# Kernel tuning notes

Hardware: AMD Instinct MI355X
Metric: run time of the kernel (lower is better)

Reference implementation:

```python
import jax, jax.numpy as jnp
import numpy as np

N, E, D, H, G = 50000, 800000, 256, 256, 64
EPS = 1e-5

def setup_inputs() -> dict:
    key = jax.random.key(0)
    ks = jax.random.split(key, 16)
    s_in = float(np.sqrt(2.0 / D))   # He fan_in init
    s_h = float(np.sqrt(2.0 / H))
    inp = {}
    inp['x'] = jax.random.normal(ks[0], (N, D), jnp.float32)
    inp['edge_index'] = jax.random.randint(ks[1], (2, E), 0, N)
    inp['batch'] = jnp.sort(jax.random.randint(ks[2], (N,), 0, G))
    inp['bn_in_g'] = jnp.ones((D,), jnp.float32)
    inp['bn_in_b'] = jnp.zeros((D,), jnp.float32)
    for i in range(3):
        fan = D if i == 0 else H
        inp[f'W{i}'] = jax.random.normal(ks[3 + i], (fan, H), jnp.float32) * float(np.sqrt(2.0 / fan))
        inp[f'b{i}'] = jnp.zeros((H,), jnp.float32)
        inp[f'bn{i}_g'] = jnp.ones((H,), jnp.float32)
        inp[f'bn{i}_b'] = jnp.zeros((H,), jnp.float32)
    inp['Wa1'] = jax.random.normal(ks[6], (H, H // 2), jnp.float32) * s_h
    inp['ba1'] = jnp.zeros((H // 2,), jnp.float32)
    inp['Wa2'] = jax.random.normal(ks[7], (H // 2, 1), jnp.float32) * float(np.sqrt(2.0 / (H // 2)))
    inp['ba2'] = jnp.zeros((1,), jnp.float32)
    inp['Wo'] = jax.random.normal(ks[8], (H, 2), jnp.float32) * s_h
    inp['bo'] = jnp.zeros((2,), jnp.float32)
    return inp


def _bn(x, g, b):
    # BatchNorm1d, batch statistics (training-mode normalization), biased var
    m = jnp.mean(x, axis=0)
    v = jnp.mean(jnp.square(x - m), axis=0)
    return (x - m) * jax.lax.rsqrt(v + EPS) * g + b


def _gcn(x, src, dst, W, b):
    h = x @ W  # [N, H]
    n = x.shape[0]
    deg = jax.ops.segment_sum(jnp.ones_like(src, x.dtype), dst, num_segments=n) + 1.0  # +1 self-loop
    dinv = jax.lax.rsqrt(deg)  # [N]
    msg = h[src] * (dinv[src] * dinv[dst])[:, None]          # gather + edgewise scale
    agg = jax.ops.segment_sum(msg, dst, num_segments=n)      # scatter-add at dst
    return agg + h * (dinv * dinv)[:, None] + b               # self-loop term fused


def reference(x, edge_index, batch, bn_in_g, bn_in_b,
              W0, b0, bn0_g, bn0_b, W1, b1, bn1_g, bn1_b, W2, b2, bn2_g, bn2_b,
              Wa1, ba1, Wa2, ba2, Wo, bo):
    src, dst = edge_index[0], edge_index[1]
    x = _bn(x, bn_in_g, bn_in_b)  # dropout = identity (eval)
    # layer 0
    xp = _bn(jax.nn.relu(_gcn(x, src, dst, W0, b0)), bn0_g, bn0_b)
    # layers 1..2 with residual
    for (W, b, g, bb) in ((W1, b1, bn1_g, bn1_b), (W2, b2, bn2_g, bn2_b)):
        xn = _bn(jax.nn.relu(_gcn(xp, src, dst, W, b)), g, bb)
        xp = xn + xp
    # attention over all nodes (softmax along node dim, as in source)
    scores = jax.nn.leaky_relu(xp @ Wa1 + ba1, 0.01) @ Wa2 + ba2  # [N,1]
    w = jax.nn.softmax(scores, axis=0)
    xw = xp * w
    cnt = jax.ops.segment_sum(jnp.ones((xp.shape[0],), xp.dtype), batch, num_segments=G)
    pooled = jax.ops.segment_sum(xw, batch, num_segments=G) / jnp.maximum(cnt, 1.0)[:, None]
    return pooled @ Wo + bo  # [G, 2]
```

## Files before the change

kernel.cpp:

```cpp
#include <hip/hip_runtime.h>

#define N_NODES 50000
#define N_EDGES 800000
#define DIM 256
#define NG 64
#define EPS_BN 1e-5f
#define NB_AGG 3125
#define NB_COL 512
#define NSPLIT 32

typedef _Float16 f16;
typedef _Float16 half8 __attribute__((ext_vector_type(8)));
typedef _Float16 half4 __attribute__((ext_vector_type(4)));
typedef float floatx4 __attribute__((ext_vector_type(4)));

__global__ __launch_bounds__(256) void col_stats_kernel(const float* __restrict__ X, int n,
                                                        float* __restrict__ part) {
    int c = threadIdx.x;
    float s = 0.f, q = 0.f;
    for (int i = blockIdx.x; i < n; i += gridDim.x) {
        float v = X[(size_t)i * DIM + c];
        s += v; q += v * v;
    }
    part[(size_t)blockIdx.x * 512 + c] = s;
    part[(size_t)blockIdx.x * 512 + DIM + c] = q;
}

__global__ __launch_bounds__(256) void reduce_stats_kernel(const float* __restrict__ part, int nrows,
                                                           float* __restrict__ p2) {
    int col = blockIdx.x * 256 + threadIdx.x;
    int chunk = (nrows + NSPLIT - 1) / NSPLIT;
    int r0 = blockIdx.y * chunk;
    int r1 = min(r0 + chunk, nrows);
    float t = 0.f;
    for (int r = r0; r < r1; r++) t += part[(size_t)r * 512 + col];
    p2[(size_t)blockIdx.y * 512 + col] = t;
}

__global__ void finalize_stats_kernel(const float* __restrict__ p2, float* __restrict__ mr, float inv_n) {
    int c = threadIdx.x;
    float s = 0.f, q = 0.f;
#pragma unroll
    for (int r = 0; r < NSPLIT; r++) {
        s += p2[(size_t)r * 512 + c];
        q += p2[(size_t)r * 512 + DIM + c];
    }
    float m = s * inv_n;
    float v = q * inv_n - m * m;
    mr[c] = m;
    mr[DIM + c] = rsqrtf(v + EPS_BN);
}

__global__ __launch_bounds__(256) void bn_apply_in_kernel(const float* __restrict__ Xin, f16* __restrict__ Af,
                                                          const float* __restrict__ mr, const float* __restrict__ g,
                                                          const float* __restrict__ b, int n) {
    int c = threadIdx.x;
    float mean = mr[c], rstd = mr[DIM + c], gg = g[c], bb = b[c];
    for (int i = blockIdx.x; i < n; i += gridDim.x) {
        size_t idx = (size_t)i * DIM + c;
        float v = Xin[idx];
        v = (v - mean) * rstd * gg + bb;
        Af[idx] = (f16)v;
    }
}

__global__ __launch_bounds__(256) void bn_apply_kernel(const f16* __restrict__ Cin, f16* __restrict__ Af,
                                                       const float* __restrict__ mr, const float* __restrict__ g,
                                                       const float* __restrict__ b, int n, int residual) {
    int c = threadIdx.x;
    float mean = mr[c], rstd = mr[DIM + c], gg = g[c], bb = b[c];
    for (int i = blockIdx.x; i < n; i += gridDim.x) {
        size_t idx = (size_t)i * DIM + c;
        float v = (float)Cin[idx];
        v = fmaxf(v, 0.f);
        v = (v - mean) * rstd * gg + bb;
        if (residual) v += (float)Af[idx];
        Af[idx] = (f16)v;
    }
}

__global__ void convert_wT_kernel(const float* __restrict__ W, f16* __restrict__ Wt, int K, int M) {
    int idx = blockIdx.x * 256 + threadIdx.x;
    if (idx < K * M) {
        int m = idx / K, k = idx % K;
        Wt[idx] = (f16)W[(size_t)k * M + m];
    }
}

__global__ void count_int_kernel(const int* __restrict__ idx, int n, int* __restrict__ cnt) {
    for (int i = blockIdx.x * blockDim.x + threadIdx.x; i < n; i += gridDim.x * blockDim.x)
        atomicAdd(&cnt[idx[i]], 1);
}

#define SCHUNK 2048
__global__ __launch_bounds__(256) void scan1_kernel(const int* __restrict__ cnt, int n,
                                                    int* __restrict__ outp, int* __restrict__ bsums,
                                                    float* __restrict__ dinv) {
    __shared__ int lds[256];
    int t = threadIdx.x;
    int base = blockIdx.x * SCHUNK + t * 8;
    int v[8]; int s = 0;
#pragma unroll
    for (int j = 0; j < 8; j++) {
        int id = base + j;
        int x = 0;
        if (id < n) { x = cnt[id]; dinv[id] = rsqrtf((float)x + 1.0f); }
        v[j] = s; s += x;
    }
    lds[t] = s; __syncthreads();
    for (int o = 1; o < 256; o <<= 1) {
        int add = (t >= o) ? lds[t - o] : 0;
        __syncthreads();
        lds[t] += add;
        __syncthreads();
    }
    int excl = lds[t] - s;
#pragma unroll
    for (int j = 0; j < 8; j++) { int id = base + j; if (id < n) outp[id] = excl + v[j]; }
    if (t == 255) bsums[blockIdx.x] = lds[255];
}

__global__ void scan2_kernel(int* bsums, int nb) {
    if (threadIdx.x == 0 && blockIdx.x == 0) {
        int r = 0;
        for (int i = 0; i < nb; i++) { int t = bsums[i]; bsums[i] = r; r += t; }
    }
}

__global__ void scan3_kernel(int* __restrict__ outp, const int* __restrict__ bsums, int n, int total) {
    int i = blockIdx.x * blockDim.x + threadIdx.x;
    if (i < n) outp[i] += bsums[i / SCHUNK];
    if (i == 0) outp[n] = total;
}

__global__ void scatter_kernel(const int* __restrict__ src, const int* __restrict__ dst, int ne,
                               const int* __restrict__ rowp, int* __restrict__ fill, int* __restrict__ ss) {
    for (int e = blockIdx.x * blockDim.x + threadIdx.x; e < ne; e += gridDim.x * blockDim.x) {
        int d = dst[e];
        int pos = rowp[d] + atomicAdd(&fill[d], 1);
        ss[pos] = src[e];
    }
}

__global__ void graph_bounds_kernel(const int* __restrict__ batch, int n, int* __restrict__ start) {
    int i = blockIdx.x * blockDim.x + threadIdx.x;
    if (i < n) {
        int b = batch[i];
        if (i == 0 || batch[i - 1] != b) start[b] = i;
    }
}

__global__ void graph_offsets2_kernel(const int* __restrict__ start, int* __restrict__ off, int* __restrict__ cnt) {
    if (threadIdx.x == 0 && blockIdx.x == 0) {
        int nxt = N_NODES;
        for (int g = NG - 1; g >= 0; --g) {
            int s = start[g];
            int o = (s < 0) ? nxt : s;
            off[g] = o;
            cnt[g] = nxt - o;
            nxt = o;
        }
    }
}

__global__ __launch_bounds__(256) void gcn_agg_kernel(const f16* __restrict__ h, const int* __restrict__ rowp,
                                                      const int* __restrict__ ss, const float* __restrict__ dinv,
                                                      const float* __restrict__ bias, f16* __restrict__ out,
                                                      float* __restrict__ part, int n) {
    int wave = threadIdx.x >> 6;
    int lane = threadIdx.x & 63;
    int c = lane * 4;
    float4 bv = *(const float4*)&bias[c];
    float s0 = 0.f, s1 = 0.f, s2 = 0.f, s3 = 0.f;
    float q0 = 0.f, q1 = 0.f, q2 = 0.f, q3 = 0.f;
    for (int row = blockIdx.x * 4 + wave; row < n; row += gridDim.x * 4) {
        float ax = 0.f, ay = 0.f, az = 0.f, aw = 0.f;
        int e0 = rowp[row], e1 = rowp[row + 1];
        int e = e0;
        for (; e + 3 < e1; e += 4) {
            int i0 = ss[e], i1 = ss[e + 1], i2 = ss[e + 2], i3 = ss[e + 3];
            half4 h0 = *(const half4*)&h[(size_t)i0 * DIM + c];
            half4 h1 = *(const half4*)&h[(size_t)i1 * DIM + c];
            half4 h2 = *(const half4*)&h[(size_t)i2 * DIM + c];
            half4 h3 = *(const half4*)&h[(size_t)i3 * DIM + c];
            ax += (float)h0[0] + (float)h1[0] + (float)h2[0] + (float)h3[0];
            ay += (float)h0[1] + (float)h1[1] + (float)h2[1] + (float)h3[1];
            az += (float)h0[2] + (float)h1[2] + (float)h2[2] + (float)h3[2];
            aw += (float)h0[3] + (float)h1[3] + (float)h2[3] + (float)h3[3];
        }
        for (; e < e1; e++) {
            int si = ss[e];
            half4 hv = *(const half4*)&h[(size_t)si * DIM + c];
            ax += (float)hv[0]; ay += (float)hv[1]; az += (float)hv[2]; aw += (float)hv[3];
        }
        float di = dinv[row];
        half4 hs = *(const half4*)&h[(size_t)row * DIM + c];
        float rx = di * (ax + (float)hs[0]) + bv.x;
        float ry = di * (ay + (float)hs[1]) + bv.y;
        float rz = di * (az + (float)hs[2]) + bv.z;
        float rw = di * (aw + (float)hs[3]) + bv.w;
        half4 o; o[0] = (f16)rx; o[1] = (f16)ry; o[2] = (f16)rz; o[3] = (f16)rw;
        *(half4*)&out[(size_t)row * DIM + c] = o;
        float t;
        t = fmaxf(rx, 0.f); s0 += t; q0 += t * t;
        t = fmaxf(ry, 0.f); s1 += t; q1 += t * t;
        t = fmaxf(rz, 0.f); s2 += t; q2 += t * t;
        t = fmaxf(rw, 0.f); s3 += t; q3 += t * t;
    }
    __shared__ float sred[4][64][4];
    __shared__ float qred[4][64][4];
    sred[wave][lane][0] = s0; sred[wave][lane][1] = s1; sred[wave][lane][2] = s2; sred[wave][lane][3] = s3;
    qred[wave][lane][0] = q0; qred[wave][lane][1] = q1; qred[wave][lane][2] = q2; qred[wave][lane][3] = q3;
    __syncthreads();
    if (wave == 0) {
        size_t base = (size_t)blockIdx.x * 512;
        float4 a = make_float4(0.f, 0.f, 0.f, 0.f), qv = make_float4(0.f, 0.f, 0.f, 0.f);
#pragma unroll
        for (int ww = 0; ww < 4; ww++) {
            a.x += sred[ww][lane][0]; a.y += sred[ww][lane][1]; a.z += sred[ww][lane][2]; a.w += sred[ww][lane][3];
            qv.x += qred[ww][lane][0]; qv.y += qred[ww][lane][1]; qv.z += qred[ww][lane][2]; qv.w += qred[ww][lane][3];
        }
        *(float4*)&part[base + c] = a;
        *(float4*)&part[base + DIM + c] = qv;
    }
}

#define BM 128
#define BN 128
#define BK 32
#define LDP 40
__global__ __launch_bounds__(256) void gemm_f16_kernel(const f16* __restrict__ Af, const f16* __restrict__ Wt,
                                                       f16* __restrict__ C, const float* __restrict__ scale,
                                                       int n, int K, int M) {
    __shared__ __align__(16) f16 As[BM * LDP];
    __shared__ __align__(16) f16 Bs[BN * LDP];
    int tid = threadIdx.x;
    int wave = tid >> 6, lane = tid & 63;
    int wm = wave >> 1, wn = wave & 1;
    int q = lane >> 4, l16 = lane & 15;
    int bm = blockIdx.x * BM, bn = blockIdx.y * BN;
    floatx4 acc[4][4] = {};
    for (int k0 = 0; k0 < K; k0 += BK) {
#pragma unroll
        for (int rr = 0; rr < 2; rr++) {
            int cidx = tid + rr * 256;
            int row = cidx >> 2, off = (cidx & 3) * 8;
            int arow = bm + row; if (arow >= n) arow = n - 1;
            *(float4*)&As[row * LDP + off] = *(const float4*)&Af[(size_t)arow * K + k0 + off];
            int brow = bn + row;
            *(float4*)&Bs[row * LDP + off] = *(const float4*)&Wt[(size_t)brow * K + k0 + off];
        }
        __syncthreads();
        half8 af[4], bf[4];
#pragma unroll
        for (int i = 0; i < 4; i++) af[i] = *(half8*)&As[(wm * 64 + i * 16 + l16) * LDP + q * 8];
#pragma unroll
        for (int j = 0; j < 4; j++) bf[j] = *(half8*)&Bs[(wn * 64 + j * 16 + l16) * LDP + q * 8];
#pragma unroll
        for (int i = 0; i < 4; i++)
#pragma unroll
            for (int j = 0; j < 4; j++)
                acc[i][j] = __builtin_amdgcn_mfma_f32_16x16x32_f16(af[i], bf[j], acc[i][j], 0, 0, 0);
        __syncthreads();
    }
#pragma unroll
    for (int i = 0; i < 4; i++) {
#pragma unroll
        for (int r = 0; r < 4; r++) {
            int row = bm + wm * 64 + i * 16 + q * 4 + r;
            if (row < n) {
                float sc = scale ? scale[row] : 1.0f;
#pragma unroll
                for (int j = 0; j < 4; j++) {
                    int col = bn + wn * 64 + j * 16 + l16;
                    C[(size_t)row * M + col] = (f16)(acc[i][j][r] * sc);
                }
            }
        }
    }
}

__global__ __launch_bounds__(256) void gemm_attn_kernel(const f16* __restrict__ Af, const f16* __restrict__ Wt,
                                                        const float* __restrict__ ba1, const float* __restrict__ Wa2,
                                                        const float* __restrict__ ba2, float* __restrict__ score,
                                                        int n, int K) {
    __shared__ __align__(16) f16 As[BM * LDP];
    __shared__ __align__(16) f16 Bs[128 * LDP];
    __shared__ float scred[128][2];
    int tid = threadIdx.x;
    int wave = tid >> 6, lane = tid & 63;
    int wm = wave >> 1, wn = wave & 1;
    int q = lane >> 4, l16 = lane & 15;
    int bm = blockIdx.x * BM;
    floatx4 acc[4][4] = {};
    for (int k0 = 0; k0 < K; k0 += BK) {
#pragma unroll
        for (int rr = 0; rr < 2; rr++) {
            int cidx = tid + rr * 256;
            int row = cidx >> 2, off = (cidx & 3) * 8;
            int arow = bm + row; if (arow >= n) arow = n - 1;
            *(float4*)&As[row * LDP + off] = *(const float4*)&Af[(size_t)arow * K + k0 + off];
            *(float4*)&Bs[row * LDP + off] = *(const float4*)&Wt[(size_t)row * K + k0 + off];
        }
        __syncthreads();
        half8 af[4], bf[4];
#pragma unroll
        for (int i = 0; i < 4; i++) af[i] = *(half8*)&As[(wm * 64 + i * 16 + l16) * LDP + q * 8];
#pragma unroll
        for (int j = 0; j < 4; j++) bf[j] = *(half8*)&Bs[(wn * 64 + j * 16 + l16) * LDP + q * 8];
#pragma unroll
        for (int i = 0; i < 4; i++)
#pragma unroll
            for (int j = 0; j < 4; j++)
                acc[i][j] = __builtin_amdgcn_mfma_f32_16x16x32_f16(af[i], bf[j], acc[i][j], 0, 0, 0);
        __syncthreads();
    }
    float ba1v[4], wa2v[4];
#pragma unroll
    for (int j = 0; j < 4; j++) {
        int col = wn * 64 + j * 16 + l16;
        ba1v[j] = ba1[col];
        wa2v[j] = Wa2[col];
    }
#pragma unroll
    for (int i = 0; i < 4; i++)
#pragma unroll
        for (int r = 0; r < 4; r++) {
            float p = 0.f;
#pragma unroll
            for (int j = 0; j < 4; j++) {
                float v = acc[i][j][r] + ba1v[j];
                v = (v > 0.f) ? v : 0.01f * v;
                p += v * wa2v[j];
            }
#pragma unroll
            for (int o = 1; o < 16; o <<= 1) p += __shfl_xor(p, o);
            if (l16 == 0) scred[wm * 64 + i * 16 + q * 4 + r][wn] = p;
        }
    __syncthreads();
    if (tid < 128) {
        int grow = bm + tid;
        if (grow < n) score[grow] = scred[tid][0] + scred[tid][1] + ba2[0];
    }
}

__global__ __launch_bounds__(256) void reduce_max_kernel(const float* __restrict__ s, int n, float* __restrict__ part) {
    __shared__ float lds[256];
    float m = -3.0e38f;
    for (int i = blockIdx.x * 256 + threadIdx.x; i < n; i += gridDim.x * 256) m = fmaxf(m, s[i]);
    lds[threadIdx.x] = m; __syncthreads();
    for (int o = 128; o > 0; o >>= 1) {
        if (threadIdx.x < o) lds[threadIdx.x] = fmaxf(lds[threadIdx.x], lds[threadIdx.x + o]);
        __syncthreads();
    }
    if (threadIdx.x == 0) part[blockIdx.x] = lds[0];
}

__global__ __launch_bounds__(256) void reduce_sumexp_kernel(const float* __restrict__ s, int n,
                                                            const float* __restrict__ part_max,
                                                            float* __restrict__ part_sum) {
    __shared__ float lds[256];
    int t = threadIdx.x;
    lds[t] = part_max[t]; __syncthreads();
    for (int o = 128; o > 0; o >>= 1) {
        if (t < o) lds[t] = fmaxf(lds[t], lds[t + o]);
        __syncthreads();
    }
    float mx = lds[0];
    __syncthreads();
    float acc = 0.f;
    for (int i = blockIdx.x * 256 + t; i < n; i += gridDim.x * 256) acc += expf(s[i] - mx);
    lds[t] = acc; __syncthreads();
    for (int o = 128; o > 0; o >>= 1) {
        if (t < o) lds[t] += lds[t + o];
        __syncthreads();
    }
    if (t == 0) part_sum[blockIdx.x] = lds[0];
}

__global__ __launch_bounds__(256) void pool_kernel(const f16* __restrict__ Af, const float* __restrict__ score,
                                                   const int* __restrict__ offs, const int* __restrict__ cnts,
                                                   const float* __restrict__ part_max, float* __restrict__ pooled) {
    __shared__ float lds[256];
    int c = threadIdx.x;
    lds[c] = part_max[c]; __syncthreads();
    for (int o = 128; o > 0; o >>= 1) {
        if (c < o) lds[c] = fmaxf(lds[c], lds[c + o]);
        __syncthreads();
    }
    float mx = lds[0];
    int g = blockIdx.x;
    int st = offs[g], cn = cnts[g];
    float acc = 0.f;
    for (int i = (int)blockIdx.y; i < cn; i += 32) {
        int i1 = i + 8, i2 = i + 16, i3 = i + 24;
        float s0 = score[st + i];
        float s1 = (i1 < cn) ? score[st + i1] : -3.0e38f;
        float s2 = (i2 < cn) ? score[st + i2] : -3.0e38f;
        float s3 = (i3 < cn) ? score[st + i3] : -3.0e38f;
        float a0 = (float)Af[(size_t)(st + i) * DIM + c];
        float a1 = (i1 < cn) ? (float)Af[(size_t)(st + i1) * DIM + c] : 0.f;
        float a2 = (i2 < cn) ? (float)Af[(size_t)(st + i2) * DIM + c] : 0.f;
        float a3 = (i3 < cn) ? (float)Af[(size_t)(st + i3) * DIM + c] : 0.f;
        acc += a0 * expf(s0 - mx) + a1 * expf(s1 - mx) + a2 * expf(s2 - mx) + a3 * expf(s3 - mx);
    }
    atomicAdd(&pooled[g * DIM + c], acc);
}

__global__ __launch_bounds__(256) void out_kernel(const float* __restrict__ pooled, const int* __restrict__ cnt,
                                                  const float* __restrict__ part_sum, const float* __restrict__ Wo,
                                                  const float* __restrict__ bo, float* __restrict__ out) {
    __shared__ float l0[256], l1[256];
    int g = blockIdx.x, c = threadIdx.x;
    l0[c] = part_sum[c]; __syncthreads();
    for (int o = 128; o > 0; o >>= 1) {
        if (c < o) l0[c] += l0[c + o];
        __syncthreads();
    }
    float denom = l0[0];
    __syncthreads();
    float scale = 1.f / (denom * fmaxf((float)cnt[g], 1.f));
    float v = pooled[g * DIM + c] * scale;
    l0[c] = v * Wo[c * 2];
    l1[c] = v * Wo[c * 2 + 1];
    __syncthreads();
    for (int o = 128; o > 0; o >>= 1) {
        if (c < o) { l0[c] += l0[c + o]; l1[c] += l1[c + o]; }
        __syncthreads();
    }
    if (c == 0) { out[g * 2] = l0[0] + bo[0]; out[g * 2 + 1] = l1[0] + bo[1]; }
}

extern "C" void kernel_launch(void* const* d_in, const int* in_sizes, int n_in,
                              void* d_out, int out_size, void* d_ws, size_t ws_size,
                              hipStream_t stream) {
    const float* x       = (const float*)d_in[0];
    const int*   ei      = (const int*)d_in[1];
    const int*   batch   = (const int*)d_in[2];
    const float* bn_in_g = (const float*)d_in[3];
    const float* bn_in_b = (const float*)d_in[4];
    const float* Ws[3]   = {(const float*)d_in[5],  (const float*)d_in[9],  (const float*)d_in[13]};
    const float* bs[3]   = {(const float*)d_in[6],  (const float*)d_in[10], (const float*)d_in[14]};
    const float* gs[3]   = {(const float*)d_in[7],  (const float*)d_in[11], (const float*)d_in[15]};
    const float* bbs[3]  = {(const float*)d_in[8],  (const float*)d_in[12], (const float*)d_in[16]};
    const float* Wa1 = (const float*)d_in[17];
    const float* ba1 = (const float*)d_in[18];
    const float* Wa2 = (const float*)d_in[19];
    const float* ba2 = (const float*)d_in[20];
    const float* Wo  = (const float*)d_in[21];
    const float* bo  = (const float*)d_in[22];

    char* w = (char*)d_ws;
    size_t off = 0;
    auto alloc = [&](size_t bytes) -> void* {
        void* p = w + off;
        off += (bytes + 255) & ~(size_t)255;
        return p;
    };
    int*   deg     = (int*)alloc((size_t)N_NODES * 4);
    int*   fill    = (int*)alloc((size_t)N_NODES * 4);
    float* pooled  = (float*)alloc((size_t)NG * DIM * 4);
    size_t zero_span = off;
    float* stats_part = (float*)alloc((size_t)NB_AGG * 512 * 4);
    float* stats_p2   = (float*)alloc((size_t)NSPLIT * 512 * 4);
    f16*   Afh  = (f16*)alloc((size_t)N_NODES * DIM * 2);
    f16*   Bh   = (f16*)alloc((size_t)N_NODES * DIM * 2);
    f16*   Ch   = (f16*)alloc((size_t)N_NODES * DIM * 2);
    f16*   Wt[3];
    for (int l = 0; l < 3; l++) Wt[l] = (f16*)alloc((size_t)DIM * DIM * 2);
    f16*   Wa1t = (f16*)alloc((size_t)128 * DIM * 2);
    int* sorted_src = (int*)alloc((size_t)N_EDGES * 4);
    float* dinv = (float*)alloc((size_t)N_NODES * 4);
    int* rowp   = (int*)alloc((size_t)(N_NODES + 1) * 4);
    float* score = (float*)alloc((size_t)N_NODES * 4);
    float* mr    = (float*)alloc(512 * 4);
    int* bsums   = (int*)alloc(64 * 4);
    float* part_max = (float*)alloc(256 * 4);
    float* part_sum = (float*)alloc(256 * 4);
    int* gstart  = (int*)alloc(64 * 4);
    int* cnt_g   = (int*)alloc(64 * 4);
    int* off_g   = (int*)alloc(64 * 4);

    const int* src = ei;
    const int* dst = ei + N_EDGES;
    const int NSCAN = (N_NODES + SCHUNK - 1) / SCHUNK;

    hipMemsetAsync(d_ws, 0, zero_span, stream);
    hipMemsetAsync(gstart, 0xff, 64 * 4, stream);

    count_int_kernel<<<3125, 256, 0, stream>>>(dst, N_EDGES, deg);
    scan1_kernel<<<NSCAN, 256, 0, stream>>>(deg, N_NODES, rowp, bsums, dinv);
    scan2_kernel<<<1, 64, 0, stream>>>(bsums, NSCAN);
    scan3_kernel<<<(N_NODES + 255) / 256, 256, 0, stream>>>(rowp, bsums, N_NODES, N_EDGES);
    scatter_kernel<<<3125, 256, 0, stream>>>(src, dst, N_EDGES, rowp, fill, sorted_src);

    graph_bounds_kernel<<<(N_NODES + 255) / 256, 256, 0, stream>>>(batch, N_NODES, gstart);
    graph_offsets2_kernel<<<1, 64, 0, stream>>>(gstart, off_g, cnt_g);

    for (int l = 0; l < 3; l++)
        convert_wT_kernel<<<DIM * DIM / 256, 256, 0, stream>>>(Ws[l], Wt[l], DIM, DIM);
    convert_wT_kernel<<<128 * DIM / 256, 256, 0, stream>>>(Wa1, Wa1t, DIM, 128);

    col_stats_kernel<<<NB_COL, 256, 0, stream>>>(x, N_NODES, stats_part);
    reduce_stats_kernel<<<dim3(2, NSPLIT), 256, 0, stream>>>(stats_part, NB_COL, stats_p2);
    finalize_stats_kernel<<<1, 256, 0, stream>>>(stats_p2, mr, 1.f / N_NODES);
    bn_apply_in_kernel<<<1024, 256, 0, stream>>>(x, Afh, mr, bn_in_g, bn_in_b, N_NODES);

    dim3 ggrid((N_NODES + BM - 1) / BM, DIM / BN);
    for (int l = 0; l < 3; l++) {
        gemm_f16_kernel<<<ggrid, 256, 0, stream>>>(Afh, Wt[l], Bh, dinv, N_NODES, DIM, DIM);
        gcn_agg_kernel<<<NB_AGG, 256, 0, stream>>>(Bh, rowp, sorted_src, dinv, bs[l], Ch, stats_part, N_NODES);
        reduce_stats_kernel<<<dim3(2, NSPLIT), 256, 0, stream>>>(stats_part, NB_AGG, stats_p2);
        finalize_stats_kernel<<<1, 256, 0, stream>>>(stats_p2, mr, 1.f / N_NODES);
        bn_apply_kernel<<<1024, 256, 0, stream>>>(Ch, Afh, mr, gs[l], bbs[l], N_NODES, (l > 0) ? 1 : 0);
    }

    gemm_attn_kernel<<<(N_NODES + BM - 1) / BM, 256, 0, stream>>>(Afh, Wa1t, ba1, Wa2, ba2, score, N_NODES, DIM);
    reduce_max_kernel<<<256, 256, 0, stream>>>(score, N_NODES, part_max);
    reduce_sumexp_kernel<<<256, 256, 0, stream>>>(score, N_NODES, part_max, part_sum);

    pool_kernel<<<dim3(NG, 8), 256, 0, stream>>>(Afh, score, off_g, cnt_g, part_max, pooled);
    out_kernel<<<NG, 256, 0, stream>>>(pooled, cnt_g, part_sum, Wo, bo, (float*)d_out);
}
```

Before: 765.0 us.

## Fuse BN apply into GEMM prologues and collapse many small launches

The batch-norm apply (with ReLU and residual add) now runs inside the GEMM's A-tile load, so the separate bn_apply passes over the node features disappear. Stats reduction and finalize merge into one kernel that uses a last-block atomic counter, and the softmax max and sum move into the attention GEMM and the pool kernel via an atomic max key and an atomic exp-sum. Weight conversion, degree count and graph bounds each become a single launch, scan2 is folded into scan3, and the aggregation gather is unrolled by eight with readfirstlane indices. The result is fewer launches and less memory traffic, at the cost of recomputing the BN transform in every GEMM column block and relying on grid-wide atomics.

After: 743.4 us. -2.8%, faster.

```diff
diff --git a/kernel.cpp b/kernel.cpp
--- a/kernel.cpp
+++ b/kernel.cpp
@@ -14,6 +14,9 @@
 typedef _Float16 half4 __attribute__((ext_vector_type(4)));
 typedef float floatx4 __attribute__((ext_vector_type(4)));
 
+__device__ __forceinline__ int fkey(float f) { int i = __float_as_int(f); return (i >= 0) ? i : (i ^ 0x7fffffff); }
+__device__ __forceinline__ float keyf(int k) { return __int_as_float((k >= 0) ? k : (k ^ 0x7fffffff)); }
+
 __global__ __launch_bounds__(256) void col_stats_kernel(const float* __restrict__ X, int n,
                                                         float* __restrict__ part) {
     int c = threadIdx.x;
@@ -26,8 +29,10 @@
     part[(size_t)blockIdx.x * 512 + DIM + c] = q;
 }
 
-__global__ __launch_bounds__(256) void reduce_stats_kernel(const float* __restrict__ part, int nrows,
-                                                           float* __restrict__ p2) {
+__global__ __launch_bounds__(256) void reduce_finalize_kernel(const float* __restrict__ part, int nrows,
+                                                              float* __restrict__ p2, int* __restrict__ counter,
+                                                              const float* __restrict__ g, const float* __restrict__ b,
+                                                              float* __restrict__ affine, float inv_n) {
     int col = blockIdx.x * 256 + threadIdx.x;
     int chunk = (nrows + NSPLIT - 1) / NSPLIT;
     int r0 = blockIdx.y * chunk;
@@ -35,61 +40,59 @@
     float t = 0.f;
     for (int r = r0; r < r1; r++) t += part[(size_t)r * 512 + col];
     p2[(size_t)blockIdx.y * 512 + col] = t;
-}
-
-__global__ void finalize_stats_kernel(const float* __restrict__ p2, float* __restrict__ mr, float inv_n) {
-    int c = threadIdx.x;
-    float s = 0.f, q = 0.f;
-#pragma unroll
-    for (int r = 0; r < NSPLIT; r++) {
-        s += p2[(size_t)r * 512 + c];
-        q += p2[(size_t)r * 512 + DIM + c];
-    }
-    float m = s * inv_n;
-    float v = q * inv_n - m * m;
-    mr[c] = m;
-    mr[DIM + c] = rsqrtf(v + EPS_BN);
-}
-
-__global__ __launch_bounds__(256) void bn_apply_in_kernel(const float* __restrict__ Xin, f16* __restrict__ Af,
-                                                          const float* __restrict__ mr, const float* __restrict__ g,
-                                                          const float* __restrict__ b, int n) {
-    int c = threadIdx.x;
-    float mean = mr[c], rstd = mr[DIM + c], gg = g[c], bb = b[c];
-    for (int i = blockIdx.x; i < n; i += gridDim.x) {
-        size_t idx = (size_t)i * DIM + c;
-        float v = Xin[idx];
-        v = (v - mean) * rstd * gg + bb;
-        Af[idx] = (f16)v;
-    }
-}
-
-__global__ __launch_bounds__(256) void bn_apply_kernel(const f16* __restrict__ Cin, f16* __restrict__ Af,
-                                                       const float* __restrict__ mr, const float* __restrict__ g,
-                                                       const float* __restrict__ b, int n, int residual) {
-    int c = threadIdx.x;
-    float mean = mr[c], rstd = mr[DIM + c], gg = g[c], bb = b[c];
-    for (int i = blockIdx.x; i < n; i += gridDim.x) {
-        size_t idx = (size_t)i * DIM + c;
-        float v = (float)Cin[idx];
-        v = fmaxf(v, 0.f);
-        v = (v - mean) * rstd * gg + bb;
-        if (residual) v += (float)Af[idx];
-        Af[idx] = (f16)v;
-    }
-}
-
-__global__ void convert_wT_kernel(const float* __restrict__ W, f16* __restrict__ Wt, int K, int M) {
+    __threadfence();
+    __shared__ int lastf;
+    if (threadIdx.x == 0) lastf = (atomicAdd(counter, 1) == 2 * NSPLIT - 1) ? 1 : 0;
+    __syncthreads();
+    if (lastf) {
+        __threadfence();
+        int c = threadIdx.x;
+        float s = 0.f, q = 0.f;
+#pragma unroll
+        for (int r = 0; r < NSPLIT; r++) {
+            s += p2[(size_t)r * 512 + c];
+            q += p2[(size_t)r * 512 + DIM + c];
+        }
+        float m = s * inv_n;
+        float v = q * inv_n - m * m;
+        float rstd = rsqrtf(v + EPS_BN);
+        float A = rstd * g[c];
+        affine[c] = A;
+        affine[DIM + c] = b[c] - m * A;
+    }
+}
+
+__global__ void convert_all_kernel(const float* __restrict__ W0, const float* __restrict__ W1,
+                                   const float* __restrict__ W2, const float* __restrict__ Wa1,
+                                   f16* __restrict__ T0, f16* __restrict__ T1,
+                                   f16* __restrict__ T2, f16* __restrict__ T3) {
     int idx = blockIdx.x * 256 + threadIdx.x;
-    if (idx < K * M) {
-        int m = idx / K, k = idx % K;
-        Wt[idx] = (f16)W[(size_t)k * M + m];
-    }
-}
-
-__global__ void count_int_kernel(const int* __restrict__ idx, int n, int* __restrict__ cnt) {
-    for (int i = blockIdx.x * blockDim.x + threadIdx.x; i < n; i += gridDim.x * blockDim.x)
-        atomicAdd(&cnt[idx[i]], 1);
+    if (idx < 196608) {
+        int w = idx >> 16, r = idx & 65535;
+        const float* W = (w == 0) ? W0 : (w == 1) ? W1 : W2;
+        f16* T = (w == 0) ? T0 : (w == 1) ? T1 : T2;
+        int m = r >> 8, k = r & 255;
+        T[r] = (f16)W[(size_t)k * 256 + m];
+    } else {
+        int r = idx - 196608;
+        int m = r >> 8, k = r & 255;
+        T3[r] = (f16)Wa1[(size_t)k * 128 + m];
+    }
+}
+
+__global__ void count_bounds_kernel(const int* __restrict__ dst, int ne, int* __restrict__ cnt,
+                                    const int* __restrict__ batch, int n, int* __restrict__ start) {
+    int gb = blockIdx.x;
+    if (gb < NB_AGG) {
+        for (int i = gb * 256 + threadIdx.x; i < ne; i += NB_AGG * 256)
+            atomicAdd(&cnt[dst[i]], 1);
+    } else {
+        int i = (gb - NB_AGG) * 256 + threadIdx.x;
+        if (i < n) {
+            int b = batch[i];
+            if (i == 0 || batch[i - 1] != b) start[b] = i;
+        }
+    }
 }
 
 #define SCHUNK 2048
@@ -120,16 +123,14 @@
     if (t == 255) bsums[blockIdx.x] = lds[255];
 }
 
-__global__ void scan2_kernel(int* bsums, int nb) {
-    if (threadIdx.x == 0 && blockIdx.x == 0) {
-        int r = 0;
-        for (int i = 0; i < nb; i++) { int t = bsums[i]; bsums[i] = r; r += t; }
-    }
-}
-
 __global__ void scan3_kernel(int* __restrict__ outp, const int* __restrict__ bsums, int n, int total) {
     int i = blockIdx.x * blockDim.x + threadIdx.x;
-    if (i < n) outp[i] += bsums[i / SCHUNK];
+    if (i < n) {
+        int k = i / SCHUNK;
+        int pref = 0;
+        for (int j = 0; j < k; j++) pref += bsums[j];
+        outp[i] += pref;
+    }
     if (i == 0) outp[n] = total;
 }
 
@@ -142,15 +143,8 @@
     }
 }
 
-__global__ void graph_bounds_kernel(const int* __restrict__ batch, int n, int* __restrict__ start) {
-    int i = blockIdx.x * blockDim.x + threadIdx.x;
-    if (i < n) {
-        int b = batch[i];
-        if (i == 0 || batch[i - 1] != b) start[b] = i;
-    }
-}
-
-__global__ void graph_offsets2_kernel(const int* __restrict__ start, int* __restrict__ off, int* __restrict__ cnt) {
+__global__ void graph_offsets2_kernel(const int* __restrict__ start, int* __restrict__ off, int* __restrict__ cnt,
+                                      int* __restrict__ maxkey) {
     if (threadIdx.x == 0 && blockIdx.x == 0) {
         int nxt = N_NODES;
         for (int g = NG - 1; g >= 0; --g) {
@@ -160,6 +154,7 @@
             cnt[g] = nxt - o;
             nxt = o;
         }
+        maxkey[0] = 0x80000000;
     }
 }
 
@@ -171,46 +166,61 @@
     int lane = threadIdx.x & 63;
     int c = lane * 4;
     float4 bv = *(const float4*)&bias[c];
-    float s0 = 0.f, s1 = 0.f, s2 = 0.f, s3 = 0.f;
-    float q0 = 0.f, q1 = 0.f, q2 = 0.f, q3 = 0.f;
+    float s0a = 0.f, s1a = 0.f, s2a = 0.f, s3a = 0.f;
+    float q0a = 0.f, q1a = 0.f, q2a = 0.f, q3a = 0.f;
     for (int row = blockIdx.x * 4 + wave; row < n; row += gridDim.x * 4) {
         float ax = 0.f, ay = 0.f, az = 0.f, aw = 0.f;
         int e0 = rowp[row], e1 = rowp[row + 1];
         int e = e0;
-        for (; e + 3 < e1; e += 4) {
-            int i0 = ss[e], i1 = ss[e + 1], i2 = ss[e + 2], i3 = ss[e + 3];
-            half4 h0 = *(const half4*)&h[(size_t)i0 * DIM + c];
-            half4 h1 = *(const half4*)&h[(size_t)i1 * DIM + c];
-            half4 h2 = *(const half4*)&h[(size_t)i2 * DIM + c];
-            half4 h3 = *(const half4*)&h[(size_t)i3 * DIM + c];
-            ax += (float)h0[0] + (float)h1[0] + (float)h2[0] + (float)h3[0];
-            ay += (float)h0[1] + (float)h1[1] + (float)h2[1] + (float)h3[1];
-            az += (float)h0[2] + (float)h1[2] + (float)h2[2] + (float)h3[2];
-            aw += (float)h0[3] + (float)h1[3] + (float)h2[3] + (float)h3[3];
+        for (; e + 8 <= e1; e += 8) {
+            int i0 = __builtin_amdgcn_readfirstlane(ss[e + 0]);
+            int i1 = __builtin_amdgcn_readfirstlane(ss[e + 1]);
+            int i2 = __builtin_amdgcn_readfirstlane(ss[e + 2]);
+            int i3 = __builtin_amdgcn_readfirstlane(ss[e + 3]);
+            int i4 = __builtin_amdgcn_readfirstlane(ss[e + 4]);
+            int i5 = __builtin_amdgcn_readfirstlane(ss[e + 5]);
+            int i6 = __builtin_amdgcn_readfirstlane(ss[e + 6]);
+            int i7 = __builtin_amdgcn_readfirstlane(ss[e + 7]);
+            half4 v0 = *(const half4*)&h[((size_t)i0 << 8) + c];
+            half4 v1 = *(const half4*)&h[((size_t)i1 << 8) + c];
+            half4 v2 = *(const half4*)&h[((size_t)i2 << 8) + c];
+            half4 v3 = *(const half4*)&h[((size_t)i3 << 8) + c];
+            half4 v4 = *(const half4*)&h[((size_t)i4 << 8) + c];
+            half4 v5 = *(const half4*)&h[((size_t)i5 << 8) + c];
+            half4 v6 = *(const half4*)&h[((size_t)i6 << 8) + c];
+            half4 v7 = *(const half4*)&h[((size_t)i7 << 8) + c];
+            ax += ((float)v0[0] + (float)v1[0]) + ((float)v2[0] + (float)v3[0]) +
+                  ((float)v4[0] + (float)v5[0]) + ((float)v6[0] + (float)v7[0]);
+            ay += ((float)v0[1] + (float)v1[1]) + ((float)v2[1] + (float)v3[1]) +
+                  ((float)v4[1] + (float)v5[1]) + ((float)v6[1] + (float)v7[1]);
+            az += ((float)v0[2] + (float)v1[2]) + ((float)v2[2] + (float)v3[2]) +
+                  ((float)v4[2] + (float)v5[2]) + ((float)v6[2] + (float)v7[2]);
+            aw += ((float)v0[3] + (float)v1[3]) + ((float)v2[3] + (float)v3[3]) +
+                  ((float)v4[3] + (float)v5[3]) + ((float)v6[3] + (float)v7[3]);
         }
         for (; e < e1; e++) {
-            int si = ss[e];
-            half4 hv = *(const half4*)&h[(size_t)si * DIM + c];
+            int si = __builtin_amdgcn_readfirstlane(ss[e]);
+            half4 hv = *(const half4*)&h[((size_t)si << 8) + c];
             ax += (float)hv[0]; ay += (float)hv[1]; az += (float)hv[2]; aw += (float)hv[3];
         }
         float di = dinv[row];
-        half4 hs = *(const half4*)&h[(size_t)row * DIM + c];
+        half4 hs = *(const half4*)&h[((size_t)row << 8) + c];
         float rx = di * (ax + (float)hs[0]) + bv.x;
         float ry = di * (ay + (float)hs[1]) + bv.y;
         float rz = di * (az + (float)hs[2]) + bv.z;
         float rw = di * (aw + (float)hs[3]) + bv.w;
         half4 o; o[0] = (f16)rx; o[1] = (f16)ry; o[2] = (f16)rz; o[3] = (f16)rw;
-        *(half4*)&out[(size_t)row * DIM + c] = o;
+        *(half4*)&out[((size_t)row << 8) + c] = o;
         float t;
-        t = fmaxf(rx, 0.f); s0 += t; q0 += t * t;
-        t = fmaxf(ry, 0.f); s1 += t; q1 += t * t;
-        t = fmaxf(rz, 0.f); s2 += t; q2 += t * t;
-        t = fmaxf(rw, 0.f); s3 += t; q3 += t * t;
+        t = fmaxf(rx, 0.f); s0a += t; q0a += t * t;
+        t = fmaxf(ry, 0.f); s1a += t; q1a += t * t;
+        t = fmaxf(rz, 0.f); s2a += t; q2a += t * t;
+        t = fmaxf(rw, 0.f); s3a += t; q3a += t * t;
     }
     __shared__ float sred[4][64][4];
     __shared__ float qred[4][64][4];
-    sred[wave][lane][0] = s0; sred[wave][lane][1] = s1; sred[wave][lane][2] = s2; sred[wave][lane][3] = s3;
-    qred[wave][lane][0] = q0; qred[wave][lane][1] = q1; qred[wave][lane][2] = q2; qred[wave][lane][3] = q3;
+    sred[wave][lane][0] = s0a; sred[wave][lane][1] = s1a; sred[wave][lane][2] = s2a; sred[wave][lane][3] = s3a;
+    qred[wave][lane][0] = q0a; qred[wave][lane][1] = q1a; qred[wave][lane][2] = q2a; qred[wave][lane][3] = q3a;
     __syncthreads();
     if (wave == 0) {
         size_t base = (size_t)blockIdx.x * 512;
@@ -229,38 +239,69 @@
 #define BN 128
 #define BK 32
 #define LDP 40
-__global__ __launch_bounds__(256) void gemm_f16_kernel(const f16* __restrict__ Af, const f16* __restrict__ Wt,
-                                                       f16* __restrict__ C, const float* __restrict__ scale,
-                                                       int n, int K, int M) {
+__global__ __launch_bounds__(256) void gemm_fused_kernel(const float* __restrict__ Xf32, const f16* __restrict__ Ch,
+                                                         const f16* __restrict__ Aold, f16* __restrict__ Afout,
+                                                         const float* __restrict__ affine,
+                                                         const f16* __restrict__ Wt, f16* __restrict__ Cout,
+                                                         const float* __restrict__ scale, int n, int K, int M) {
     __shared__ __align__(16) f16 As[BM * LDP];
     __shared__ __align__(16) f16 Bs[BN * LDP];
+    __shared__ float sA[256], sB[256];
     int tid = threadIdx.x;
+    if (tid < 256) { sA[tid] = affine[tid]; sB[tid] = affine[256 + tid]; }
     int wave = tid >> 6, lane = tid & 63;
     int wm = wave >> 1, wn = wave & 1;
     int q = lane >> 4, l16 = lane & 15;
     int bm = blockIdx.x * BM, bn = blockIdx.y * BN;
+    int kc = (tid & 3) * 8;
+    int writer = (Afout != nullptr) && (blockIdx.y == 0);
     floatx4 acc[4][4] = {};
+    __syncthreads();
     for (int k0 = 0; k0 < K; k0 += BK) {
+        float a8[8], b8[8];
+#pragma unroll
+        for (int j = 0; j < 8; j++) { a8[j] = sA[k0 + kc + j]; b8[j] = sB[k0 + kc + j]; }
 #pragma unroll
         for (int rr = 0; rr < 2; rr++) {
             int cidx = tid + rr * 256;
-            int row = cidx >> 2, off = (cidx & 3) * 8;
+            int row = cidx >> 2;
             int arow = bm + row; if (arow >= n) arow = n - 1;
-            *(float4*)&As[row * LDP + off] = *(const float4*)&Af[(size_t)arow * K + k0 + off];
+            float v[8];
+            if (Xf32) {
+                float4 x0 = *(const float4*)&Xf32[(size_t)arow * K + k0 + kc];
+                float4 x1 = *(const float4*)&Xf32[(size_t)arow * K + k0 + kc + 4];
+                v[0] = x0.x; v[1] = x0.y; v[2] = x0.z; v[3] = x0.w;
+                v[4] = x1.x; v[5] = x1.y; v[6] = x1.z; v[7] = x1.w;
+            } else {
+                half8 ch = *(const half8*)&Ch[(size_t)arow * K + k0 + kc];
+#pragma unroll
+                for (int j = 0; j < 8; j++) v[j] = fmaxf((float)ch[j], 0.f);
+            }
+            half8 af;
+            if (Aold) {
+                half8 ao = *(const half8*)&Aold[(size_t)arow * K + k0 + kc];
+#pragma unroll
+                for (int j = 0; j < 8; j++) af[j] = (f16)(v[j] * a8[j] + b8[j] + (float)ao[j]);
+            } else {
+#pragma unroll
+                for (int j = 0; j < 8; j++) af[j] = (f16)(v[j] * a8[j] + b8[j]);
+            }
+            *(float4*)&As[row * LDP + kc] = *(float4*)&af;
+            if (writer && bm + row < n) *(half8*)&Afout[(size_t)arow * K + k0 + kc] = af;
             int brow = bn + row;
-            *(float4*)&Bs[row * LDP + off] = *(const float4*)&Wt[(size_t)brow * K + k0 + off];
-        }
-        __syncthreads();
-        half8 af[4], bf[4];
-#pragma unroll
-        for (int i = 0; i < 4; i++) af[i] = *(half8*)&As[(wm * 64 + i * 16 + l16) * LDP + q * 8];
-#pragma unroll
-        for (int j = 0; j < 4; j++) bf[j] = *(half8*)&Bs[(wn * 64 + j * 16 + l16) * LDP + q * 8];
+            *(float4*)&Bs[row * LDP + kc] = *(const float4*)&Wt[(size_t)brow * K + k0 + kc];
+        }
+        __syncthreads();
+        half8 afr[4], bfr[4];
+#pragma unroll
+        for (int i = 0; i < 4; i++) afr[i] = *(half8*)&As[(wm * 64 + i * 16 + l16) * LDP + q * 8];
+#pragma unroll
+        for (int j = 0; j < 4; j++) bfr[j] = *(half8*)&Bs[(wn * 64 + j * 16 + l16) * LDP + q * 8];
 #pragma unroll
         for (int i = 0; i < 4; i++)
 #pragma unroll
             for (int j = 0; j < 4; j++)
-                acc[i][j] = __builtin_amdgcn_mfma_f32_16x16x32_f16(af[i], bf[j], acc[i][j], 0, 0, 0);
+                acc[i][j] = __builtin_amdgcn_mfma_f32_16x16x32_f16(afr[i], bfr[j], acc[i][j], 0, 0, 0);
         __syncthreads();
     }
 #pragma unroll
@@ -269,50 +310,66 @@
         for (int r = 0; r < 4; r++) {
             int row = bm + wm * 64 + i * 16 + q * 4 + r;
             if (row < n) {
-                float sc = scale ? scale[row] : 1.0f;
+                float sc = scale[row];
 #pragma unroll
                 for (int j = 0; j < 4; j++) {
                     int col = bn + wn * 64 + j * 16 + l16;
-                    C[(size_t)row * M + col] = (f16)(acc[i][j][r] * sc);
+                    Cout[(size_t)row * M + col] = (f16)(acc[i][j][r] * sc);
                 }
             }
         }
     }
 }
 
-__global__ __launch_bounds__(256) void gemm_attn_kernel(const f16* __restrict__ Af, const f16* __restrict__ Wt,
+__global__ __launch_bounds__(256) void gemm_attn_kernel(const f16* __restrict__ Ch, const f16* __restrict__ Aold,
+                                                        f16* __restrict__ Afout, const float* __restrict__ affine,
+                                                        const f16* __restrict__ Wt,
                                                         const float* __restrict__ ba1, const float* __restrict__ Wa2,
                                                         const float* __restrict__ ba2, float* __restrict__ score,
-                                                        int n, int K) {
+                                                        int* __restrict__ maxkey, int n, int K) {
     __shared__ __align__(16) f16 As[BM * LDP];
     __shared__ __align__(16) f16 Bs[128 * LDP];
+    __shared__ float sA[256], sB[256];
     __shared__ float scred[128][2];
     int tid = threadIdx.x;
+    if (tid < 256) { sA[tid] = affine[tid]; sB[tid] = affine[256 + tid]; }
     int wave = tid >> 6, lane = tid & 63;
     int wm = wave >> 1, wn = wave & 1;
     int q = lane >> 4, l16 = lane & 15;
     int bm = blockIdx.x * BM;
+    int kc = (tid & 3) * 8;
     floatx4 acc[4][4] = {};
+    __syncthreads();
     for (int k0 = 0; k0 < K; k0 += BK) {
+        float a8[8], b8[8];
+#pragma unroll
+        for (int j = 0; j < 8; j++) { a8[j] = sA[k0 + kc + j]; b8[j] = sB[k0 + kc + j]; }
 #pragma unroll
         for (int rr = 0; rr < 2; rr++) {
             int cidx = tid + rr * 256;
-            int row = cidx >> 2, off = (cidx & 3) * 8;
+            int row = cidx >> 2;
             int arow = bm + row; if (arow >= n) arow = n - 1;
-            *(float4*)&As[row * LDP + off] = *(const float4*)&Af[(size_t)arow * K + k0 + off];
-            *(float4*)&Bs[row * LDP + off] = *(const float4*)&Wt[(size_t)row * K + k0 + off];
-        }
-        __syncthreads();
-        half8 af[4], bf[4];
-#pragma unroll
-        for (int i = 0; i < 4; i++) af[i] = *(half8*)&As[(wm * 64 + i * 16 + l16) * LDP + q * 8];
-#pragma unroll
-        for (int j = 0; j < 4; j++) bf[j] = *(half8*)&Bs[(wn * 64 + j * 16 + l16) * LDP + q * 8];
+            half8 ch = *(const half8*)&Ch[(size_t)arow * K + k0 + kc];
+            half8 ao = *(const half8*)&Aold[(size_t)arow * K + k0 + kc];
+            half8 af;
+#pragma unroll
+            for (int j = 0; j < 8; j++)
+                af[j] = (f16)(fmaxf((float)ch[j], 0.f) * a8[j] + b8[j] + (float)ao[j]);
+            *(float4*)&As[row * LDP + kc] = *(float4*)&af;
+            if (bm + row < n) *(half8*)&Afout[(size_t)arow * K + k0 + kc] = af;
+            *(float4*)&Bs[row * LDP + kc] = *(const float4*)&Wt[(size_t)row * K + k0 + kc];
+        }
+        __syncthreads();
+        half8 afr[4], bfr[4];
+#pragma unroll
+        for (int i = 0; i < 4; i++) afr[i] = *(half8*)&As[(wm * 64 + i * 16 + l16) * LDP + q * 8];
+#pragma unroll
+        for (int j = 0; j < 4; j++) bfr[j] = *(half8*)&Bs[(wn * 64 + j * 16 + l16) * LDP + q * 8];
 #pragma unroll
         for (int i = 0; i < 4; i++)
 #pragma unroll
             for (int j = 0; j < 4; j++)
-                acc[i][j] = __builtin_amdgcn_mfma_f32_16x16x32_f16(af[i], bf[j], acc[i][j], 0, 0, 0);
+                acc[i][j] = __builtin_amdgcn_mfma_f32_16x16x32_f16(afr[i], bfr[j], acc[i][j], 0, 0, 0);
         __syncthreads();
     }
     float ba1v[4], wa2v[4];
@@ -338,88 +395,54 @@
             if (l16 == 0) scred[wm * 64 + i * 16 + q * 4 + r][wn] = p;
         }
     __syncthreads();
+    __shared__ float mred[128];
     if (tid < 128) {
         int grow = bm + tid;
-        if (grow < n) score[grow] = scred[tid][0] + scred[tid][1] + ba2[0];
-    }
-}
-
-__global__ __launch_bounds__(256) void reduce_max_kernel(const float* __restrict__ s, int n, float* __restrict__ part) {
-    __shared__ float lds[256];
-    float m = -3.0e38f;
-    for (int i = blockIdx.x * 256 + threadIdx.x; i < n; i += gridDim.x * 256) m = fmaxf(m, s[i]);
-    lds[threadIdx.x] = m; __syncthreads();
-    for (int o = 128; o > 0; o >>= 1) {
-        if (threadIdx.x < o) lds[threadIdx.x] = fmaxf(lds[threadIdx.x], lds[threadIdx.x + o]);
-        __syncthreads();
-    }
-    if (threadIdx.x == 0) part[blockIdx.x] = lds[0];
-}
-
-__global__ __launch_bounds__(256) void reduce_sumexp_kernel(const float* __restrict__ s, int n,
-                                                            const float* __restrict__ part_max,
-                                                            float* __restrict__ part_sum) {
-    __shared__ float lds[256];
-    int t = threadIdx.x;
-    lds[t] = part_max[t]; __syncthreads();
-    for (int o = 128; o > 0; o >>= 1) {
-        if (t < o) lds[t] = fmaxf(lds[t], lds[t + o]);
-        __syncthreads();
-    }
-    float mx = lds[0];
-    __syncthreads();
-    float acc = 0.f;
-    for (int i = blockIdx.x * 256 + t; i < n; i += gridDim.x * 256) acc += expf(s[i] - mx);
-    lds[t] = acc; __syncthreads();
-    for (int o = 128; o > 0; o >>= 1) {
-        if (t < o) lds[t] += lds[t + o];
-        __syncthreads();
-    }
-    if (t == 0) part_sum[blockIdx.x] = lds[0];
+        float sc = scred[tid][0] + scred[tid][1] + ba2[0];
+        if (grow < n) score[grow] = sc; else sc = -3.0e38f;
+        mred[tid] = sc;
+    }
+    __syncthreads();
+    for (int o = 64; o > 0; o >>= 1) {
+        if (tid < o && tid + o < 128) mred[tid] = fmaxf(mred[tid], mred[tid + o]);
+        __syncthreads();
+    }
+    if (tid == 0) atomicMax(maxkey, fkey(mred[0]));
 }
 
 __global__ __launch_bounds__(256) void pool_kernel(const f16* __restrict__ Af, const float* __restrict__ score,
                                                    const int* __restrict__ offs, const int* __restrict__ cnts,
-                                                   const float* __restrict__ part_max, float* __restrict__ pooled) {
-    __shared__ float lds[256];
+                                                   const int* __restrict__ maxkey, float* __restrict__ expsum,
+                                                   float* __restrict__ pooled) {
+    float mx = keyf(maxkey[0]);
     int c = threadIdx.x;
-    lds[c] = part_max[c]; __syncthreads();
-    for (int o = 128; o > 0; o >>= 1) {
-        if (c < o) lds[c] = fmaxf(lds[c], lds[c + o]);
-        __syncthreads();
-    }
-    float mx = lds[0];
     int g = blockIdx.x;
     int st = offs[g], cn = cnts[g];
-    float acc = 0.f;
+    float acc = 0.f, esum = 0.f;
     for (int i = (int)blockIdx.y; i < cn; i += 32) {
         int i1 = i + 8, i2 = i + 16, i3 = i + 24;
         float s0 = score[st + i];
         float s1 = (i1 < cn) ? score[st + i1] : -3.0e38f;
         float s2 = (i2 < cn) ? score[st + i2] : -3.0e38f;
         float s3 = (i3 < cn) ? score[st + i3] : -3.0e38f;
+        float e0 = expf(s0 - mx), e1 = expf(s1 - mx), e2 = expf(s2 - mx), e3 = expf(s3 - mx);
         float a0 = (float)Af[(size_t)(st + i) * DIM + c];
         float a1 = (i1 < cn) ? (float)Af[(size_t)(st + i1) * DIM + c] : 0.f;
         float a2 = (i2 < cn) ? (float)Af[(size_t)(st + i2) * DIM + c] : 0.f;
         float a3 = (i3 < cn) ? (float)Af[(size_t)(st + i3) * DIM + c] : 0.f;
-        acc += a0 * expf(s0 - mx) + a1 * expf(s1 - mx) + a2 * expf(s2 - mx) + a3 * expf(s3 - mx);
+        acc += a0 * e0 + a1 * e1 + a2 * e2 + a3 * e3;
+        esum += (e0 + e1) + (e2 + e3);
     }
     atomicAdd(&pooled[g * DIM + c], acc);
+    if (c == 0) atomicAdd(expsum, esum);
 }
 
 __global__ __launch_bounds__(256) void out_kernel(const float* __restrict__ pooled, const int* __restrict__ cnt,
-                                                  const float* __restrict__ part_sum, const float* __restrict__ Wo,
+                                                  const float* __restrict__ expsum, const float* __restrict__ Wo,
                                                   const float* __restrict__ bo, float* __restrict__ out) {
     __shared__ float l0[256], l1[256];
     int g = blockIdx.x, c = threadIdx.x;
-    l0[c] = part_sum[c]; __syncthreads();
-    for (int o = 128; o > 0; o >>= 1) {
-        if (c < o) l0[c] += l0[c + o];
-        __syncthreads();
-    }
-    float denom = l0[0];
-    __syncthreads();
-    float scale = 1.f / (denom * fmaxf((float)cnt[g], 1.f));
+    float scale = 1.f / (expsum[0] * fmaxf((float)cnt[g], 1.f));
     float v = pooled[g * DIM + c] * scale;
     l0[c] = v * Wo[c * 2];
     l1[c] = v * Wo[c * 2 + 1];
@@ -460,12 +483,16 @@
     int*   deg     = (int*)alloc((size_t)N_NODES * 4);
     int*   fill    = (int*)alloc((size_t)N_NODES * 4);
     float* pooled  = (float*)alloc((size_t)NG * DIM * 4);
+    int*   counters = (int*)alloc(4 * 4);
+    float* expsum  = (float*)alloc(4);
     size_t zero_span = off;
     float* stats_part = (float*)alloc((size_t)NB_AGG * 512 * 4);
     float* stats_p2   = (float*)alloc((size_t)NSPLIT * 512 * 4);
-    f16*   Afh  = (f16*)alloc((size_t)N_NODES * DIM * 2);
+    float* affine  = (float*)alloc(512 * 4);
+    f16*   AfA  = (f16*)alloc((size_t)N_NODES * DIM * 2);
+    f16*   AfB  = (f16*)alloc((size_t)N_NODES * DIM * 2);
     f16*   Bh   = (f16*)alloc((size_t)N_NODES * DIM * 2);
-    f16*   Ch   = (f16*)alloc((size_t)N_NODES * DIM * 2);
+    f16*   Chb  = (f16*)alloc((size_t)N_NODES * DIM * 2);
     f16*   Wt[3];
     for (int l = 0; l < 3; l++) Wt[l] = (f16*)alloc((size_t)DIM * DIM * 2);
     f16*   Wa1t = (f16*)alloc((size_t)128 * DIM * 2);
@@ -473,10 +500,8 @@
     float* dinv = (float*)alloc((size_t)N_NODES * 4);
     int* rowp   = (int*)alloc((size_t)(N_NODES + 1) * 4);
     float* score = (float*)alloc((size_t)N_NODES * 4);
-    float* mr    = (float*)alloc(512 * 4);
     int* bsums   = (int*)alloc(64 * 4);
-    float* part_max = (float*)alloc(256 * 4);
-    float* part_sum = (float*)alloc(256 * 4);
+    int* maxkey  = (int*)alloc(16);
     int* gstart  = (int*)alloc(64 * 4);
     int* cnt_g   = (int*)alloc(64 * 4);
     int* off_g   = (int*)alloc(64 * 4);
@@ -484,41 +509,40 @@
     const int* src = ei;
     const int* dst = ei + N_EDGES;
     const int NSCAN = (N_NODES + SCHUNK - 1) / SCHUNK;
+    const float inv_n = 1.f / N_NODES;
 
     hipMemsetAsync(d_ws, 0, zero_span, stream);
     hipMemsetAsync(gstart, 0xff, 64 * 4, stream);
 
-    count_int_kernel<<<3125, 256, 0, stream>>>(dst, N_EDGES, deg);
+    count_bounds_kernel<<<NB_AGG + 196, 256, 0, stream>>>(dst, N_EDGES, deg, batch, N_NODES, gstart);
     scan1_kernel<<<NSCAN, 256, 0, stream>>>(deg, N_NODES, rowp, bsums, dinv);
-    scan2_kernel<<<1, 64, 0, stream>>>(bsums, NSCAN);
     scan3_kernel<<<(N_NODES + 255) / 256, 256, 0, stream>>>(rowp, bsums, N_NODES, N_EDGES);
-    scatter_kernel<<<3125, 256, 0, stream>>>(src, dst, N_EDGES, rowp, fill, sorted_src);
-
-    graph_bounds_kernel<<<(N_NODES + 255) / 256, 256, 0, stream>>>(batch, N_NODES, gstart);
-    graph_offsets2_kernel<<<1, 64, 0, stream>>>(gstart, off_g, cnt_g);
-
-    for (int l = 0; l < 3; l++)
-        convert_wT_kernel<<<DIM * DIM / 256, 256, 0, stream>>>(Ws[l], Wt[l], DIM, DIM);
-    convert_wT_kernel<<<128 * DIM / 256, 256, 0, stream>>>(Wa1, Wa1t, DIM, 128);
+    scatter_kernel<<<NB_AGG, 256, 0, stream>>>(src, dst, N_EDGES, rowp, fill, sorted_src);
+    graph_offsets2_kernel<<<1, 64, 0, stream>>>(gstart, off_g, cnt_g, maxkey);
+
+    convert_all_kernel<<<896, 256, 0, stream>>>(Ws[0], Ws[1], Ws[2], Wa1, Wt[0], Wt[1], Wt[2], Wa1t);
 
     col_stats_kernel<<<NB_COL, 256, 0, stream>>>(x, N_NODES, stats_part);
-    reduce_stats_kernel<<<dim3(2, NSPLIT), 256, 0, stream>>>(stats_part, NB_COL, stats_p2);
-    finalize_stats_kernel<<<1, 256, 0, stream>>>(stats_p2, mr, 1.f / N_NODES);
-    bn_apply_in_kernel<<<1024, 256, 0, stream>>>(x, Afh, mr, bn_in_g, bn_in_b, N_NODES);
+    reduce_finalize_kernel<<<dim3(2, NSPLIT), 256, 0, stream>>>(stats_part, NB_COL, stats_p2, counters + 0,
+                                                                bn_in_g, bn_in_b, affine, inv_n);
 
     dim3 ggrid((N_NODES + BM - 1) / BM, DIM / BN);
-    for (int l = 0; l < 3; l++) {
-        gemm_f16_kernel<<<ggrid, 256, 0, stream>>>(Afh, Wt[l], Bh, dinv, N_NODES, DIM, DIM);
-        gcn_agg_kernel<<<NB_AGG, 256, 0, stream>>>(Bh, rowp, sorted_src, dinv, bs[l], Ch, stats_part, N_NODES);
-        reduce_stats_kernel<<<dim3(2, NSPLIT), 256, 0, stream>>>(stats_part, NB_AGG, stats_p2);
-        finalize_stats_kernel<<<1, 256, 0, stream>>>(stats_p2, mr, 1.f / N_NODES);
-        bn_apply_kernel<<<1024, 256, 0, stream>>>(Ch, Afh, mr, gs[l], bbs[l], N_NODES, (l > 0) ? 1 : 0);
-    }
-
-    gemm_attn_kernel<<<(N_NODES + BM - 1) / BM, 256, 0, stream>>>(Afh, Wa1t, ba1, Wa2, ba2, score, N_NODES, DIM);
-    reduce_max_kernel<<<256, 256, 0, stream>>>(score, N_NODES, part_max);
-    reduce_sumexp_kernel<<<256, 256, 0, stream>>>(score, N_NODES, part_max, part_sum);
-
-    pool_kernel<<<dim3(NG, 8), 256, 0, stream>>>(Afh, score, off_g, cnt_g, part_max, pooled);
-    out_kernel<<<NG, 256, 0, stream>>>(pooled, cnt_g, part_sum, Wo, bo, (float*)d_out);
-}
+    gemm_fused_kernel<<<ggrid, 256, 0, stream>>>(x, nullptr, nullptr, nullptr, affine, Wt[0], Bh, dinv, N_NODES, DIM, DIM);
+    gcn_agg_kernel<<<NB_AGG, 256, 0, stream>>>(Bh, rowp, sorted_src, dinv, bs[0], Chb, stats_part, N_NODES);
+    reduce_finalize_kernel<<<dim3(2, NSPLIT), 256, 0, stream>>>(stats_part, NB_AGG, stats_p2, counters + 1,
+                                                                gs[0], bbs[0], affine, inv_n);
+    gemm_fused_kernel<<<ggrid, 256, 0, stream>>>(nullptr, Chb, nullptr, AfA, affine, Wt[1], Bh, dinv, N_NODES, DIM, DIM);
+    gcn_agg_kernel<<<NB_AGG, 256, 0, stream>>>(Bh, rowp, sorted_src, dinv, bs[1], Chb, stats_part, N_NODES);
+    reduce_finalize_kernel<<<dim3(2, NSPLIT), 256, 0, stream>>>(stats_part, NB_AGG, stats_p2, counters + 2,
+                                                                gs[1], bbs[1], affine, inv_n);
+    gemm_fused_kernel<<<ggrid, 256, 0, stream>>>(nullptr, Chb, AfA, AfB, affine, Wt[2], Bh, dinv, N_NODES, DIM, DIM);
+    gcn_agg_kernel<<<NB_AGG, 256, 0, stream>>>(Bh, rowp, sorted_src, dinv, bs[2], Chb, stats_part, N_NODES);
+    reduce_finalize_kernel<<<dim3(2, NSPLIT), 256, 0, stream>>>(stats_part, NB_AGG, stats_p2, counters + 3,
+                                                                gs[2], bbs[2], affine, inv_n);
+
+    gemm_attn_kernel<<<(N_NODES + BM - 1) / BM, 256, 0, stream>>>(Chb, AfB, AfA, affine, Wa1t,
+                                                                  ba1, Wa2, ba2, score, maxkey, N_NODES, DIM);
+
+    pool_kernel<<<dim3(NG, 8), 256, 0, stream>>>(AfA, score, off_g, cnt_g, maxkey, expsum, pooled);
+    out_kernel<<<NG, 256, 0, stream>>>(pooled, cnt_g, expsum, Wo, bo, (float*)d_out);
+}
```
